# Optimization experiments

Hardware: AMD Instinct MI355X
Metric: run time of the kernel (lower is better)

## Reference

```python
import jax, jax.numpy as jnp
import numpy as np

N_NODES = 50000
N_EDGES = 800000
IN_F = 128
HID = 128
OUT_F = 128
NUM_LAYERS = 3


def _glorot(key, shape):
    fan_in, fan_out = shape
    lim = np.sqrt(6.0 / (fan_in + fan_out)).astype(np.float32)
    return jax.random.uniform(key, shape, jnp.float32, -lim, lim)


def setup_inputs() -> dict:
    key = jax.random.key(0)
    ks = jax.random.split(key, 12)
    x = jax.random.normal(ks[0], (N_NODES, IN_F), jnp.float32)
    edge_index = jax.random.randint(ks[1], (2, N_EDGES), 0, N_NODES, jnp.int64)
    dims = [(IN_F, HID), (HID, HID), (HID, OUT_F)]
    inp = {"x": x, "edge_index": edge_index}
    for i, (di, do) in enumerate(dims):
        inp[f"Wl{i}"] = _glorot(ks[2 + 3 * i], (di, do))      # neighbor (lin_l) weight
        inp[f"bl{i}"] = jnp.zeros((do,), jnp.float32)          # lin_l bias
        inp[f"Wr{i}"] = _glorot(ks[3 + 3 * i], (di, do))      # root (lin_r) weight, no bias
    return inp


def _sage_layer(x, src, dst, Wl, bl, Wr):
    # scatter-mean of source features onto destination nodes
    msg = x[src]                                               # [E, F] gather
    summed = jax.ops.segment_sum(msg, dst, num_segments=N_NODES)
    cnt = jax.ops.segment_sum(jnp.ones((src.shape[0],), x.dtype), dst,
                              num_segments=N_NODES)
    agg = summed / jnp.maximum(cnt, 1.0)[:, None]              # mean; 0 if no neighbors
    return agg @ Wl + bl + x @ Wr


def reference(x, edge_index, Wl0, bl0, Wr0, Wl1, bl1, Wr1, Wl2, bl2, Wr2):
    src, dst = edge_index[0], edge_index[1]
    params = [(Wl0, bl0, Wr0), (Wl1, bl1, Wr1), (Wl2, bl2, Wr2)]
    for i, (Wl, bl, Wr) in enumerate(params):
        x = _sage_layer(x, src, dst, Wl, bl, Wr)
        if i < NUM_LAYERS - 1:
            x = jax.nn.relu(x)
    return x
```

## Files before the change

kernel.cpp:

```cpp
#include <hip/hip_runtime.h>

#define F 128

typedef __attribute__((ext_vector_type(8))) short short8v;
typedef __attribute__((ext_vector_type(4))) float f32x4;

__device__ __forceinline__ unsigned short f2bf(float f) {
    unsigned int u = __builtin_bit_cast(unsigned int, f);
    unsigned int r = (u + 0x7fffu + ((u >> 16) & 1u)) >> 16;
    return (unsigned short)r;
}
__device__ __forceinline__ float bf2f(unsigned int b16) {
    unsigned int u = b16 << 16;
    return __builtin_bit_cast(float, u);
}

__global__ void detect_i64(const int* __restrict__ ei, int* __restrict__ flag) {
    __shared__ int any_nonzero;
    if (threadIdx.x == 0) any_nonzero = 0;
    __syncthreads();
    int v = ei[2 * threadIdx.x + 1];
    if (v != 0) atomicOr(&any_nonzero, 1);
    __syncthreads();
    if (threadIdx.x == 0) *flag = (any_nonzero == 0) ? 1 : 0;
}

__device__ __forceinline__ int load_src(const int* ei, int is64, int E, int e) {
    return is64 ? ei[2 * e] : ei[e];
}
__device__ __forceinline__ int load_dst(const int* ei, int is64, int E, int e) {
    return is64 ? ei[2 * (E + e)] : ei[E + e];
}

__global__ void count_rank(const int* __restrict__ ei, const int* __restrict__ flag,
                           int* __restrict__ deg, int* __restrict__ rank, int E) {
    int e = blockIdx.x * blockDim.x + threadIdx.x;
    if (e >= E) return;
    int is64 = *flag;
    int d = load_dst(ei, is64, E, e);
    rank[e] = atomicAdd(&deg[d], 1);
}

__global__ __launch_bounds__(1024) void scan_local(const int* __restrict__ deg,
                                                   int* __restrict__ rs,
                                                   int* __restrict__ partials, int N) {
    __shared__ int wsum[16];
    const int tid = threadIdx.x;
    const int lane = tid & 63, wid = tid >> 6;
    int i = blockIdx.x * 1024 + tid;
    int v = (i < N) ? deg[i] : 0;
    int incl = v;
#pragma unroll
    for (int d = 1; d < 64; d <<= 1) {
        int t = __shfl_up(incl, d);
        if (lane >= d) incl += t;
    }
    if (lane == 63) wsum[wid] = incl;
    __syncthreads();
    if (tid == 0) {
        int acc = 0;
#pragma unroll
        for (int w = 0; w < 16; ++w) { int t = wsum[w]; wsum[w] = acc; acc += t; }
        partials[blockIdx.x] = acc;
    }
    __syncthreads();
    if (i < N) rs[i] = wsum[wid] + (incl - v);
}

__global__ void scan_part(const int* __restrict__ partials, int* __restrict__ coff,
                          int nch) {
    int tid = threadIdx.x;
    int v = (tid < nch) ? partials[tid] : 0;
    int incl = v;
#pragma unroll
    for (int d = 1; d < 64; d <<= 1) {
        int t = __shfl_up(incl, d);
        if (tid >= d) incl += t;
    }
    coff[tid] = incl - v;
}

__global__ void fill_adj(const int* __restrict__ ei, const int* __restrict__ flag,
                         const int* __restrict__ rs, const int* __restrict__ coff,
                         const int* __restrict__ rank, int* __restrict__ adj, int E) {
    int e = blockIdx.x * blockDim.x + threadIdx.x;
    if (e >= E) return;
    int is64 = *flag;
    int s = load_src(ei, is64, E, e);
    int d = load_dst(ei, is64, E, e);
    adj[rs[d] + coff[d >> 10] + rank[e]] = s;
}

__global__ void convert_x(const float* __restrict__ x, unsigned short* __restrict__ xb,
                          int total) {
    int i = blockIdx.x * blockDim.x + threadIdx.x;
    if (i * 4 >= total) return;
    float4 v = *(const float4*)(x + i * 4);
    ushort4 o;
    o.x = f2bf(v.x); o.y = f2bf(v.y); o.z = f2bf(v.z); o.w = f2bf(v.w);
    *(ushort4*)(xb + i * 4) = o;
}

__global__ void convert_w(const float* __restrict__ Wl, const float* __restrict__ Wr,
                          unsigned short* __restrict__ Wpack) {
    int t = blockIdx.x * blockDim.x + threadIdx.x;
    if (t >= 4096) return;
    int lane = t & 63;
    int nt = (t >> 6) & 7;
    int kt = (t >> 9) & 7;
    int c = nt * 16 + (lane & 15);
    int kbase = kt * 32 + ((lane >> 4) << 3);
    unsigned short o[8];
#pragma unroll
    for (int i = 0; i < 8; ++i) {
        int k = kbase + i;
        float v = (k < 128) ? Wl[k * F + c] : Wr[(k - 128) * F + c];
        o[i] = f2bf(v);
    }
    *(uint4*)(Wpack + (size_t)t * 8) = *(const uint4*)o;
}

__global__ __launch_bounds__(256) void gather_mean(
    const unsigned short* __restrict__ xb, const int* __restrict__ adj,
    const int* __restrict__ rs, const int* __restrict__ coff,
    const int* __restrict__ deg, unsigned short* __restrict__ aggb, int N) {
    int n = (blockIdx.x * blockDim.x + threadIdx.x) >> 6;
    if (n >= N) return;
    const int lane = threadIdx.x & 63;
    const int half = lane >> 5, l5 = lane & 31;
    const int start = rs[n] + coff[n >> 10];
    const int d = deg[n];
    float a0 = 0.f, a1 = 0.f, a2 = 0.f, a3 = 0.f;
    int i = half;
    for (; i + 6 < d; i += 8) {
        int s0 = adj[start + i + 0];
        int s1 = adj[start + i + 2];
        int s2 = adj[start + i + 4];
        int s3 = adj[start + i + 6];
        uint2 v0 = *(const uint2*)(xb + (size_t)s0 * F + l5 * 4);
        uint2 v1 = *(const uint2*)(xb + (size_t)s1 * F + l5 * 4);
        uint2 v2 = *(const uint2*)(xb + (size_t)s2 * F + l5 * 4);
        uint2 v3 = *(const uint2*)(xb + (size_t)s3 * F + l5 * 4);
        a0 += bf2f(v0.x & 0xffff) + bf2f(v1.x & 0xffff) + bf2f(v2.x & 0xffff) + bf2f(v3.x & 0xffff);
        a1 += bf2f(v0.x >> 16) + bf2f(v1.x >> 16) + bf2f(v2.x >> 16) + bf2f(v3.x >> 16);
        a2 += bf2f(v0.y & 0xffff) + bf2f(v1.y & 0xffff) + bf2f(v2.y & 0xffff) + bf2f(v3.y & 0xffff);
        a3 += bf2f(v0.y >> 16) + bf2f(v1.y >> 16) + bf2f(v2.y >> 16) + bf2f(v3.y >> 16);
    }
    for (; i < d; i += 2) {
        int s = adj[start + i];
        uint2 v = *(const uint2*)(xb + (size_t)s * F + l5 * 4);
        a0 += bf2f(v.x & 0xffff);
        a1 += bf2f(v.x >> 16);
        a2 += bf2f(v.y & 0xffff);
        a3 += bf2f(v.y >> 16);
    }
    a0 += __shfl_xor(a0, 32);
    a1 += __shfl_xor(a1, 32);
    a2 += __shfl_xor(a2, 32);
    a3 += __shfl_xor(a3, 32);
    if (half == 0) {
        float inv = 1.0f / fmaxf((float)d, 1.0f);
        uint2 o;
        o.x = ((unsigned int)f2bf(a1 * inv) << 16) | f2bf(a0 * inv);
        o.y = ((unsigned int)f2bf(a3 * inv) << 16) | f2bf(a2 * inv);
        *(uint2*)(aggb + (size_t)n * F + l5 * 4) = o;
    }
}

__global__ __launch_bounds__(256) void sage_mfma(
    const unsigned short* __restrict__ aggb, const unsigned short* __restrict__ xb,
    const unsigned short* __restrict__ Wpack, const float* __restrict__ bl,
    unsigned short* __restrict__ outb, float* __restrict__ outf,
    int N, int final_layer) {
    const int wid = threadIdx.x >> 6;
    const int lane = threadIdx.x & 63;
    const int gw = blockIdx.x * 4 + wid;
    const int row0 = gw * 16;
    if (row0 >= N) return;

    const int rA = row0 + (lane & 15);
    const int kidx = (lane >> 4) << 3;

    f32x4 acc[8];
#pragma unroll
    for (int nt = 0; nt < 8; ++nt) acc[nt] = (f32x4){0.f, 0.f, 0.f, 0.f};

    const unsigned short* arow_a = aggb + (size_t)rA * F + kidx;
    const unsigned short* arow_x = xb + (size_t)rA * F + kidx;

#pragma unroll
    for (int kt = 0; kt < 8; ++kt) {
        const unsigned short* ap = (kt < 4) ? (arow_a + kt * 32) : (arow_x + (kt - 4) * 32);
        short8v a = *(const short8v*)ap;
#pragma unroll
        for (int nt = 0; nt < 8; ++nt) {
            short8v b = *(const short8v*)(Wpack + ((size_t)(kt * 8 + nt) * 64 + lane) * 8);
            acc[nt] = __builtin_amdgcn_mfma_f32_16x16x32_bf16(a, b, acc[nt], 0, 0, 0);
        }
    }

    const int c0 = lane & 15;
    const int r0 = row0 + ((lane >> 4) << 2);
#pragma unroll
    for (int nt = 0; nt < 8; ++nt) {
        const int col = nt * 16 + c0;
        const float b = bl[col];
#pragma unroll
        for (int reg = 0; reg < 4; ++reg) {
            const int r = r0 + reg;
            float v = acc[nt][reg] + b;
            if (!final_layer) {
                v = fmaxf(v, 0.f);
                outb[(size_t)r * F + col] = f2bf(v);
            } else {
                outf[(size_t)r * F + col] = v;
            }
        }
    }
}

extern "C" void kernel_launch(void* const* d_in, const int* in_sizes, int n_in,
                              void* d_out, int out_size, void* d_ws, size_t ws_size,
                              hipStream_t stream) {
    const float* x = (const float*)d_in[0];
    const int* ei = (const int*)d_in[1];
    const int E = in_sizes[1] / 2;
    const int N = in_sizes[0] / F;
    const int NCH = (N + 1023) / 1024;

    const float* Wl[3] = {(const float*)d_in[2], (const float*)d_in[5], (const float*)d_in[8]};
    const float* bl[3] = {(const float*)d_in[3], (const float*)d_in[6], (const float*)d_in[9]};
    const float* Wr[3] = {(const float*)d_in[4], (const float*)d_in[7], (const float*)d_in[10]};
    float* out = (float*)d_out;

    char* ws = (char*)d_ws;
    size_t off = 0;
    auto alloc = [&](size_t bytes) {
        size_t o = off;
        off = (off + bytes + 255) & ~(size_t)255;
        return o;
    };
    int* flag = (int*)(ws + alloc(4));
    int* deg = (int*)(ws + alloc((size_t)N * 4));
    int* rs = (int*)(ws + alloc((size_t)N * 4));
    int* partials = (int*)(ws + alloc(64 * 4));
    int* coff = (int*)(ws + alloc(64 * 4));
    int* rank = (int*)(ws + alloc((size_t)E * 4));
    int* adj = (int*)(ws + alloc((size_t)E * 4));
    unsigned short* xb = (unsigned short*)(ws + alloc((size_t)N * F * 2));
    unsigned short* aggb = (unsigned short*)(ws + alloc((size_t)N * F * 2));
    unsigned short* h1b = (unsigned short*)(ws + alloc((size_t)N * F * 2));
    unsigned short* h2b = (unsigned short*)(ws + alloc((size_t)N * F * 2));
    unsigned short* Wp = (unsigned short*)(ws + alloc((size_t)3 * 4096 * 8 * 2));

    detect_i64<<<1, 256, 0, stream>>>(ei, flag);
    hipMemsetAsync(deg, 0, (size_t)N * 4, stream);
    count_rank<<<(E + 255) / 256, 256, 0, stream>>>(ei, flag, deg, rank, E);
    scan_local<<<NCH, 1024, 0, stream>>>(deg, rs, partials, N);
    scan_part<<<1, 64, 0, stream>>>(partials, coff, NCH);
    fill_adj<<<(E + 255) / 256, 256, 0, stream>>>(ei, flag, rs, coff, rank, adj, E);

    convert_x<<<((N * F / 4) + 255) / 256, 256, 0, stream>>>(x, xb, N * F);
    for (int L = 0; L < 3; ++L)
        convert_w<<<16, 256, 0, stream>>>(Wl[L], Wr[L], Wp + (size_t)L * 32768);

    const unsigned short* cur = xb;
    unsigned short* hb[3] = {h1b, h2b, nullptr};
    int nblocks = ((N + 15) / 16 + 3) / 4;
    for (int layer = 0; layer < 3; ++layer) {
        gather_mean<<<(N * 64 + 255) / 256, 256, 0, stream>>>(cur, adj, rs, coff, deg, aggb, N);
        sage_mfma<<<nblocks, 256, 0, stream>>>(aggb, cur, Wp + (size_t)layer * 32768,
                                               bl[layer], hb[layer], out, N, layer == 2);
        cur = hb[layer];
    }
}
```

Baseline: 225.0 us.

## Fuse setup launches, widen gather loads, stage weights in LDS for MFMA

Folds the deg memset into the int64-detect kernel and merges x and weight conversion into one launch, cutting launch overhead. gather_mean now has each 16-lane quarter load 16-byte chunks covering a full row, so four edges are in flight per wave with fewer, wider loads. sage_mfma uses 512-thread blocks that first copy the 64KB packed weights into shared memory, so B operands come from LDS instead of global or L2. The LDS copy adds a per-block prologue and its 64KB footprint limits how many blocks fit per CU.

```diff
diff --git a/kernel.cpp b/kernel.cpp
--- a/kernel.cpp
+++ b/kernel.cpp
@@ -15,14 +15,19 @@
     return __builtin_bit_cast(float, u);
 }
 
-__global__ void detect_i64(const int* __restrict__ ei, int* __restrict__ flag) {
-    __shared__ int any_nonzero;
-    if (threadIdx.x == 0) any_nonzero = 0;
-    __syncthreads();
-    int v = ei[2 * threadIdx.x + 1];
-    if (v != 0) atomicOr(&any_nonzero, 1);
-    __syncthreads();
-    if (threadIdx.x == 0) *flag = (any_nonzero == 0) ? 1 : 0;
+__global__ void init_deg(const int* __restrict__ ei, int* __restrict__ flag,
+                         int* __restrict__ deg, int N) {
+    int i = blockIdx.x * blockDim.x + threadIdx.x;
+    if (i < N) deg[i] = 0;
+    if (blockIdx.x == 0) {
+        __shared__ int any_nonzero;
+        if (threadIdx.x == 0) any_nonzero = 0;
+        __syncthreads();
+        int v = ei[2 * threadIdx.x + 1];
+        if (v != 0) atomicOr(&any_nonzero, 1);
+        __syncthreads();
+        if (threadIdx.x == 0) *flag = (any_nonzero == 0) ? 1 : 0;
+    }
 }
 
 __device__ __forceinline__ int load_src(const int* ei, int is64, int E, int e) {
@@ -91,23 +96,29 @@
     adj[rs[d] + coff[d >> 10] + rank[e]] = s;
 }
 
-__global__ void convert_x(const float* __restrict__ x, unsigned short* __restrict__ xb,
-                          int total) {
-    int i = blockIdx.x * blockDim.x + threadIdx.x;
-    if (i * 4 >= total) return;
-    float4 v = *(const float4*)(x + i * 4);
-    ushort4 o;
-    o.x = f2bf(v.x); o.y = f2bf(v.y); o.z = f2bf(v.z); o.w = f2bf(v.w);
-    *(ushort4*)(xb + i * 4) = o;
-}
-
-__global__ void convert_w(const float* __restrict__ Wl, const float* __restrict__ Wr,
-                          unsigned short* __restrict__ Wpack) {
-    int t = blockIdx.x * blockDim.x + threadIdx.x;
-    if (t >= 4096) return;
-    int lane = t & 63;
-    int nt = (t >> 6) & 7;
-    int kt = (t >> 9) & 7;
+__global__ void convert_all(const float* __restrict__ x, unsigned short* __restrict__ xb,
+                            int nxblocks,
+                            const float* __restrict__ Wl0, const float* __restrict__ Wr0,
+                            const float* __restrict__ Wl1, const float* __restrict__ Wr1,
+                            const float* __restrict__ Wl2, const float* __restrict__ Wr2,
+                            unsigned short* __restrict__ Wp) {
+    int b = blockIdx.x;
+    if (b < nxblocks) {
+        int i = b * 256 + threadIdx.x;
+        float4 v = *(const float4*)(x + (size_t)i * 4);
+        ushort4 o;
+        o.x = f2bf(v.x); o.y = f2bf(v.y); o.z = f2bf(v.z); o.w = f2bf(v.w);
+        *(ushort4*)(xb + (size_t)i * 4) = o;
+        return;
+    }
+    int t = (b - nxblocks) * 256 + threadIdx.x;
+    int L = t >> 12;
+    int tt = t & 4095;
+    const float* Wl = (L == 0) ? Wl0 : (L == 1) ? Wl1 : Wl2;
+    const float* Wr = (L == 0) ? Wr0 : (L == 1) ? Wr1 : Wr2;
+    int lane = tt & 63;
+    int nt = (tt >> 6) & 7;
+    int kt = (tt >> 9) & 7;
     int c = nt * 16 + (lane & 15);
     int kbase = kt * 32 + ((lane >> 4) << 3);
     unsigned short o[8];
@@ -117,7 +128,7 @@
         float v = (k < 128) ? Wl[k * F + c] : Wr[(k - 128) * F + c];
         o[i] = f2bf(v);
     }
-    *(uint4*)(Wpack + (size_t)t * 8) = *(const uint4*)o;
+    *(uint4*)(Wp + ((size_t)L * 32768) + (size_t)tt * 8) = *(const uint4*)o;
 }
 
 __global__ __launch_bounds__(256) void gather_mean(
@@ -127,55 +138,76 @@
     int n = (blockIdx.x * blockDim.x + threadIdx.x) >> 6;
     if (n >= N) return;
     const int lane = threadIdx.x & 63;
-    const int half = lane >> 5, l5 = lane & 31;
+    const int q = lane >> 4, l4 = lane & 15;
     const int start = rs[n] + coff[n >> 10];
     const int d = deg[n];
+    const unsigned short* xbase = xb + l4 * 8;
     float a0 = 0.f, a1 = 0.f, a2 = 0.f, a3 = 0.f;
-    int i = half;
-    for (; i + 6 < d; i += 8) {
-        int s0 = adj[start + i + 0];
-        int s1 = adj[start + i + 2];
-        int s2 = adj[start + i + 4];
-        int s3 = adj[start + i + 6];
-        uint2 v0 = *(const uint2*)(xb + (size_t)s0 * F + l5 * 4);
-        uint2 v1 = *(const uint2*)(xb + (size_t)s1 * F + l5 * 4);
-        uint2 v2 = *(const uint2*)(xb + (size_t)s2 * F + l5 * 4);
-        uint2 v3 = *(const uint2*)(xb + (size_t)s3 * F + l5 * 4);
-        a0 += bf2f(v0.x & 0xffff) + bf2f(v1.x & 0xffff) + bf2f(v2.x & 0xffff) + bf2f(v3.x & 0xffff);
-        a1 += bf2f(v0.x >> 16) + bf2f(v1.x >> 16) + bf2f(v2.x >> 16) + bf2f(v3.x >> 16);
-        a2 += bf2f(v0.y & 0xffff) + bf2f(v1.y & 0xffff) + bf2f(v2.y & 0xffff) + bf2f(v3.y & 0xffff);
-        a3 += bf2f(v0.y >> 16) + bf2f(v1.y >> 16) + bf2f(v2.y >> 16) + bf2f(v3.y >> 16);
-    }
-    for (; i < d; i += 2) {
+    float a4 = 0.f, a5 = 0.f, a6 = 0.f, a7 = 0.f;
+    int i = q;
+    for (; i + 4 < d; i += 8) {
+        int s0 = adj[start + i];
+        int s1 = adj[start + i + 4];
+        uint4 v0 = *(const uint4*)(xbase + (size_t)s0 * F);
+        uint4 v1 = *(const uint4*)(xbase + (size_t)s1 * F);
+        a0 += bf2f(v0.x & 0xffff) + bf2f(v1.x & 0xffff);
+        a1 += bf2f(v0.x >> 16) + bf2f(v1.x >> 16);
+        a2 += bf2f(v0.y & 0xffff) + bf2f(v1.y & 0xffff);
+        a3 += bf2f(v0.y >> 16) + bf2f(v1.y >> 16);
+        a4 += bf2f(v0.z & 0xffff) + bf2f(v1.z & 0xffff);
+        a5 += bf2f(v0.z >> 16) + bf2f(v1.z >> 16);
+        a6 += bf2f(v0.w & 0xffff) + bf2f(v1.w & 0xffff);
+        a7 += bf2f(v0.w >> 16) + bf2f(v1.w >> 16);
+    }
+    if (i < d) {
         int s = adj[start + i];
-        uint2 v = *(const uint2*)(xb + (size_t)s * F + l5 * 4);
+        uint4 v = *(const uint4*)(xbase + (size_t)s * F);
         a0 += bf2f(v.x & 0xffff);
         a1 += bf2f(v.x >> 16);
         a2 += bf2f(v.y & 0xffff);
         a3 += bf2f(v.y >> 16);
-    }
-    a0 += __shfl_xor(a0, 32);
-    a1 += __shfl_xor(a1, 32);
-    a2 += __shfl_xor(a2, 32);
-    a3 += __shfl_xor(a3, 32);
-    if (half == 0) {
+        a4 += bf2f(v.z & 0xffff);
+        a5 += bf2f(v.z >> 16);
+        a6 += bf2f(v.w & 0xffff);
+        a7 += bf2f(v.w >> 16);
+    }
+    a0 += __shfl_xor(a0, 16); a0 += __shfl_xor(a0, 32);
+    a1 += __shfl_xor(a1, 16); a1 += __shfl_xor(a1, 32);
+    a2 += __shfl_xor(a2, 16); a2 += __shfl_xor(a2, 32);
+    a3 += __shfl_xor(a3, 16); a3 += __shfl_xor(a3, 32);
+    a4 += __shfl_xor(a4, 16); a4 += __shfl_xor(a4, 32);
+    a5 += __shfl_xor(a5, 16); a5 += __shfl_xor(a5, 32);
+    a6 += __shfl_xor(a6, 16); a6 += __shfl_xor(a6, 32);
+    a7 += __shfl_xor(a7, 16); a7 += __shfl_xor(a7, 32);
+    if (q == 0) {
         float inv = 1.0f / fmaxf((float)d, 1.0f);
-        uint2 o;
+        uint4 o;
         o.x = ((unsigned int)f2bf(a1 * inv) << 16) | f2bf(a0 * inv);
         o.y = ((unsigned int)f2bf(a3 * inv) << 16) | f2bf(a2 * inv);
-        *(uint2*)(aggb + (size_t)n * F + l5 * 4) = o;
-    }
-}
-
-__global__ __launch_bounds__(256) void sage_mfma(
+        o.z = ((unsigned int)f2bf(a5 * inv) << 16) | f2bf(a4 * inv);
+        o.w = ((unsigned int)f2bf(a7 * inv) << 16) | f2bf(a6 * inv);
+        *(uint4*)(aggb + (size_t)n * F + l4 * 8) = o;
+    }
+}
+
+__global__ __launch_bounds__(512) void sage_mfma(
     const unsigned short* __restrict__ aggb, const unsigned short* __restrict__ xb,
     const unsigned short* __restrict__ Wpack, const float* __restrict__ bl,
     unsigned short* __restrict__ outb, float* __restrict__ outf,
     int N, int final_layer) {
+    __shared__ unsigned short sW[32768];
+    {
+        const uint4* srcv = (const uint4*)Wpack;
+        uint4* dstv = (uint4*)sW;
+#pragma unroll
+        for (int t = 0; t < 8; ++t)
+            dstv[threadIdx.x + t * 512] = srcv[threadIdx.x + t * 512];
+    }
+    __syncthreads();
+
     const int wid = threadIdx.x >> 6;
     const int lane = threadIdx.x & 63;
-    const int gw = blockIdx.x * 4 + wid;
-    const int row0 = gw * 16;
+    const int row0 = (blockIdx.x * 8 + wid) * 16;
     if (row0 >= N) return;
 
     const int rA = row0 + (lane & 15);
@@ -194,7 +226,7 @@
         short8v a = *(const short8v*)ap;
 #pragma unroll
         for (int nt = 0; nt < 8; ++nt) {
-            short8v b = *(const short8v*)(Wpack + ((size_t)(kt * 8 + nt) * 64 + lane) * 8);
+            short8v b = *(const short8v*)(sW + ((kt * 8 + nt) * 64 + lane) * 8);
             acc[nt] = __builtin_amdgcn_mfma_f32_16x16x32_bf16(a, b, acc[nt], 0, 0, 0);
         }
     }
@@ -253,24 +285,25 @@
     unsigned short* h2b = (unsigned short*)(ws + alloc((size_t)N * F * 2));
     unsigned short* Wp = (unsigned short*)(ws + alloc((size_t)3 * 4096 * 8 * 2));
 
-    detect_i64<<<1, 256, 0, stream>>>(ei, flag);
-    hipMemsetAsync(deg, 0, (size_t)N * 4, stream);
+    init_deg<<<(N + 255) / 256, 256, 0, stream>>>(ei, flag, deg, N);
     count_rank<<<(E + 255) / 256, 256, 0, stream>>>(ei, flag, deg, rank, E);
     scan_local<<<NCH, 1024, 0, stream>>>(deg, rs, partials, N);
     scan_part<<<1, 64, 0, stream>>>(partials, coff, NCH);
     fill_adj<<<(E + 255) / 256, 256, 0, stream>>>(ei, flag, rs, coff, rank, adj, E);
 
-    convert_x<<<((N * F / 4) + 255) / 256, 256, 0, stream>>>(x, xb, N * F);
-    for (int L = 0; L < 3; ++L)
-        convert_w<<<16, 256, 0, stream>>>(Wl[L], Wr[L], Wp + (size_t)L * 32768);
+    int nxblocks = (N * F / 4 + 255) / 256;
+    convert_all<<<nxblocks + 48, 256, 0, stream>>>(x, xb, nxblocks,
+                                                   Wl[0], Wr[0], Wl[1], Wr[1], Wl[2], Wr[2],
+                                                   Wp);
 
     const unsigned short* cur = xb;
     unsigned short* hb[3] = {h1b, h2b, nullptr};
-    int nblocks = ((N + 15) / 16 + 3) / 4;
+    int nwaves = (N + 15) / 16;
+    int nblocks_m = (nwaves + 7) / 8;
     for (int layer = 0; layer < 3; ++layer) {
         gather_mean<<<(N * 64 + 255) / 256, 256, 0, stream>>>(cur, adj, rs, coff, deg, aggb, N);
-        sage_mfma<<<nblocks, 256, 0, stream>>>(aggb, cur, Wp + (size_t)layer * 32768,
-                                               bl[layer], hb[layer], out, N, layer == 2);
+        sage_mfma<<<nblocks_m, 512, 0, stream>>>(aggb, cur, Wp + (size_t)layer * 32768,
+                                                 bl[layer], hb[layer], out, N, layer == 2);
         cur = hb[layer];
     }
 }
```

New measurement: 192.0 us. 1.17x faster.
